# Kernel optimization log

Measured on AMD Instinct MI355X. Metric: run time of the kernel, lower is better.

The kernel has to match this reference:

```python
import jax, jax.numpy as jnp
import numpy as np
from jax import lax

B, T = 8, 32
D, H, W = 32, 32, 32
V = D * H * W
NPTS = 400          # nonzero events scattered per frame (<= K)
K = 512             # candidate cap (upper bound on nonzeros per frame)
DIST_THR = 2.0      # distance_threshold
MAX_EVENTS = 100    # max_events


def setup_inputs() -> dict:
    key = jax.random.key(0)
    k1, k2, k3 = jax.random.split(key, 3)
    magnitude = jax.random.normal(k1, (B, T, D, H, W), dtype=jnp.float32)
    # sparse positive energy: scatter NPTS uniform values per frame
    idx = jax.random.randint(k2, (B, T, NPTS), 0, V)
    vals = jax.random.uniform(k3, (B, T, NPTS), minval=0.1, maxval=1.0, dtype=jnp.float32)
    energy = jnp.zeros((B, T, V), jnp.float32).at[
        jnp.arange(B)[:, None, None], jnp.arange(T)[None, :, None], idx
    ].set(vals).reshape(B, T, D, H, W)
    x = jnp.stack([energy, magnitude], axis=2)  # [B,T,2,D,H,W]
    return {"x": x}


def _nms_mask(energy_flat):
    """Greedy 3D NMS over nonzero voxels of one frame. Returns keep-mask over V voxels."""
    scores, idx = lax.top_k(energy_flat, K)          # descending; all nonzeros are in top-K
    valid = scores > 0                               # top_k fill beyond nonzeros has score 0
    z = idx // (H * W)
    y = (idx // W) % H
    xx = idx % W
    coords = jnp.stack([z, y, xx], axis=-1).astype(jnp.float32)  # [K,3]
    ar = jnp.arange(K)

    def body(keep, i):
        active = keep[i] & valid[i]
        dist = jnp.sqrt(((coords[i] - coords) ** 2).sum(-1))
        suppress = active & (ar > i) & (dist < DIST_THR)
        return keep & ~suppress, None

    keep, _ = lax.scan(body, jnp.ones(K, bool), ar)
    keep = keep & valid
    # if more than max_events kept, drop everything past sorted index max_events
    keep = jnp.where(keep.sum() > MAX_EVENTS, keep & (ar < MAX_EVENTS), keep)
    mask = jnp.zeros_like(energy_flat).at[idx].add(keep.astype(energy_flat.dtype))
    return mask  # [V] in {0,1}


def _filter_frame(frame):
    # frame: [2, D, H, W]
    e = frame[0].reshape(V)
    mask = _nms_mask(e).reshape(1, D, H, W)
    has_points = jnp.any(e != 0)
    # empty frame passes through unchanged (original appends x[b,t] as-is)
    return jnp.where(has_points, frame * mask, frame)


def reference(x) -> jnp.ndarray:
    b, t = x.shape[:2]
    frames = x.reshape(b * t, 2, D, H, W)
    out = jax.vmap(_filter_frame)(frames)
    return out.reshape(x.shape)
```

## Files before the change

### kernel.cpp

```cpp
#include <hip/hip_runtime.h>
#include <stdint.h>

typedef unsigned long long u64;
typedef unsigned int u32;

#define VOX     32768
#define KCAP    512
#define MAXEV   100
#define NBRCAP  26
#define K1_BPF  8
#define K1_THREADS 256
#define K2_THREADS 512
#define CNT_STRIDE 16


__global__ __launch_bounds__(K1_THREADS) void stage_kernel(
    const float* __restrict__ x, float* __restrict__ out,
    int* __restrict__ gcnt, int* __restrict__ gnz, u64* __restrict__ grec)
{
    const int bid = blockIdx.x;
    const int f   = bid / K1_BPF;
    const int c   = bid % K1_BPF;
    const int tid = threadIdx.x;

    __shared__ u64 sbuf[KCAP];
    __shared__ int s_cnt, s_nz, s_base;

    if (tid == 0) { s_cnt = 0; s_nz = 0; }
    __syncthreads();

    {
        float4* o4 = (float4*)(out + (size_t)f * 2 * VOX) + c * (2 * VOX / K1_BPF / 4);
        const float4 z = make_float4(0.f, 0.f, 0.f, 0.f);
        #pragma unroll
        for (int h = 0; h < (2 * VOX / K1_BPF / 4) / K1_THREADS; ++h)
            o4[tid + h * K1_THREADS] = z;
    }

    const float4* e4 = (const float4*)(x + (size_t)f * 2 * VOX) + c * (VOX / K1_BPF / 4);
    bool anynz = false;
    #pragma unroll
    for (int h = 0; h < (VOX / K1_BPF / 4) / K1_THREADS; ++h) {
        int li = tid + h * K1_THREADS;
        float4 v = e4[li];
        int vbase = c * (VOX / K1_BPF) + li * 4;
        float vv[4] = {v.x, v.y, v.z, v.w};
        #pragma unroll
        for (int cc = 0; cc < 4; ++cc) {
            float val = vv[cc];
            anynz |= (val != 0.f);
            if (val > 0.f) {
                int slot = atomicAdd(&s_cnt, 1);
                if (slot < KCAP) {
                    int vox = vbase + cc;
                    sbuf[slot] = ((u64)__float_as_uint(val) << 32) | (u64)(~(u32)vox);
                }
            }
        }
    }
    if (anynz) s_nz = 1;
    __syncthreads();

    const int cnt = min(s_cnt, KCAP);
    if (tid == 0) {
        if (cnt) s_base = atomicAdd(&gcnt[f * CNT_STRIDE], cnt);
        if (s_nz) gnz[f] = 1;
    }
    __syncthreads();

    if (cnt) {
        const int base = s_base;
        for (int i = tid; i < cnt; i += K1_THREADS) {
            int o = base + i;
            if (o < KCAP) grec[f * KCAP + o] = sbuf[i];
        }
    }
}

__global__ __launch_bounds__(K2_THREADS) void nms_scatter_kernel(
    const float* __restrict__ x, float* __restrict__ out,
    const int* __restrict__ gcnt, const int* __restrict__ gnz,
    const u64* __restrict__ grec)
{
    const int f   = blockIdx.x;
    const int tid = threadIdx.x;

    __shared__ unsigned short smap[VOX];
    __shared__ u64   skey[KCAP];
    __shared__ short srank[KCAP];
    __shared__ unsigned char status[KCAP];
    __shared__ unsigned short pnbr[KCAP * NBRCAP];
    __shared__ int s_nkept, s_undec;

    const int n  = min(gcnt[f * CNT_STRIDE], KCAP);
    const int nz = gnz[f];

    if (nz == 0) {
        const float4* x4 = (const float4*)(x + (size_t)f * 2 * VOX);
        float4*       o4 = (float4*)(out + (size_t)f * 2 * VOX);
        for (int i = tid; i < 2 * VOX / 4; i += K2_THREADS) o4[i] = x4[i];
        return;
    }

    if (tid == 0) s_nkept = 0;
    {
        u32* m32 = (u32*)smap;
        #pragma unroll
        for (int h = 0; h < VOX / 2 / K2_THREADS; ++h)
            m32[tid + h * K2_THREADS] = 0xFFFFFFFFu;
    }
    __syncthreads();

    if (tid < n) {
        u64 k = grec[f * KCAP + tid];
        skey[tid] = k;
        smap[(int)(~(u32)k) & (VOX - 1)] = (unsigned short)tid;
    }
    __syncthreads();

    int pcnt = 0;
    if (tid < n) {
        const u64 kt = skey[tid];
        int rank = 0;
        #pragma unroll 8
        for (int i = 0; i < n; ++i)
            rank += (skey[i] > kt);
        srank[tid] = (short)rank;

        const int vox = (int)(~(u32)kt) & (VOX - 1);
        const int zt = vox >> 10, yt = (vox >> 5) & 31, xt = vox & 31;
        #pragma unroll
        for (int dz = -1; dz <= 1; ++dz) {
            int z = zt + dz; if ((unsigned)z >= 32) continue;
            #pragma unroll
            for (int dy = -1; dy <= 1; ++dy) {
                int yy = yt + dy; if ((unsigned)yy >= 32) continue;
                #pragma unroll
                for (int dx = -1; dx <= 1; ++dx) {
                    int xx = xt + dx; if ((unsigned)xx >= 32) continue;
                    int nv = (z << 10) | (yy << 5) | xx;
                    if (nv == vox) continue;
                    unsigned short m = smap[nv];
                    if (m != 0xFFFFu && skey[m] > kt)
                        pnbr[tid * NBRCAP + pcnt++] = m;
                }
            }
        }
        status[tid] = (pcnt == 0) ? (unsigned char)1 : (unsigned char)0;
    }
    __syncthreads();

    for (int round = 0; round < KCAP; ++round) {
        if (tid == 0) s_undec = 0;
        __syncthreads();
        if (tid < n && status[tid] == 0) {
            bool anyKept = false, anyUndec = false;
            for (int p = 0; p < pcnt; ++p) {
                unsigned char s = status[pnbr[tid * NBRCAP + p]];
                anyKept  |= (s == 1);
                anyUndec |= (s == 0);
            }
            if (anyKept)        status[tid] = 2;
            else if (!anyUndec) status[tid] = 1;
            else                s_undec = 1;
        }
        __syncthreads();
        if (s_undec == 0) break;
    }

    if (tid < n && status[tid] == 1) atomicAdd(&s_nkept, 1);
    __syncthreads();
    const int nkept = s_nkept;
    if (tid < n && status[tid] == 1 &&
        !(nkept > MAXEV && srank[tid] >= MAXEV)) {
        u64 k = skey[tid];
        int   vox = (int)(~(u32)k) & (VOX - 1);
        float val = __uint_as_float((u32)(k >> 32));
        float* of = out + (size_t)f * 2 * VOX;
        of[vox]       = val;
        of[VOX + vox] = x[(size_t)f * 2 * VOX + VOX + vox];
    }
}

extern "C" void kernel_launch(void* const* d_in, const int* in_sizes, int n_in,
                              void* d_out, int out_size, void* d_ws, size_t ws_size,
                              hipStream_t stream) {
    const float* x = (const float*)d_in[0];
    float* out = (float*)d_out;
    int frames = in_sizes[0] / (2 * VOX);

    int* gcnt = (int*)d_ws;
    int* gnz  = (int*)((char*)d_ws + 16384);
    u64* grec = (u64*)((char*)d_ws + 32768);

    hipMemsetAsync(d_ws, 0, 17408, stream);
    stage_kernel<<<frames * K1_BPF, K1_THREADS, 0, stream>>>(x, out, gcnt, gnz, grec);
    nms_scatter_kernel<<<frames, K2_THREADS, 0, stream>>>(x, out, gcnt, gnz, grec);
}
```

Baseline: 126.1 us.

## Replace global atomic compaction with per-block segments and drop memset

Each stage block now writes its candidates into a private fixed-size segment and records its own count and nonzero flag, instead of atomically reserving space in a shared per-frame buffer. The NMS kernel prefix-sums the eight segment counts and gathers segments per wavefront into shared memory. This removes the global atomics and the separate hipMemsetAsync launch. The cost is a larger workspace and a short serial prefix sum in the second kernel, and candidate order now follows block order rather than atomic arrival order.

```diff
diff --git a/kernel.cpp b/kernel.cpp
--- a/kernel.cpp
+++ b/kernel.cpp
@@ -11,7 +11,7 @@
 #define K1_BPF  8
 #define K1_THREADS 256
 #define K2_THREADS 512
-#define CNT_STRIDE 16
+#define SEGCAP  512
 
 
 __global__ __launch_bounds__(K1_THREADS) void stage_kernel(
@@ -23,8 +23,8 @@
     const int c   = bid % K1_BPF;
     const int tid = threadIdx.x;
 
-    __shared__ u64 sbuf[KCAP];
-    __shared__ int s_cnt, s_nz, s_base;
+    __shared__ u64 sbuf[SEGCAP];
+    __shared__ int s_cnt, s_nz;
 
     if (tid == 0) { s_cnt = 0; s_nz = 0; }
     __syncthreads();
@@ -51,7 +51,7 @@
             anynz |= (val != 0.f);
             if (val > 0.f) {
                 int slot = atomicAdd(&s_cnt, 1);
-                if (slot < KCAP) {
+                if (slot < SEGCAP) {
                     int vox = vbase + cc;
                     sbuf[slot] = ((u64)__float_as_uint(val) << 32) | (u64)(~(u32)vox);
                 }
@@ -61,19 +61,12 @@
     if (anynz) s_nz = 1;
     __syncthreads();
 
-    const int cnt = min(s_cnt, KCAP);
+    const int cnt = min(s_cnt, SEGCAP);
+    for (int i = tid; i < cnt; i += K1_THREADS)
+        grec[((size_t)f * K1_BPF + c) * SEGCAP + i] = sbuf[i];
     if (tid == 0) {
-        if (cnt) s_base = atomicAdd(&gcnt[f * CNT_STRIDE], cnt);
-        if (s_nz) gnz[f] = 1;
-    }
-    __syncthreads();
-
-    if (cnt) {
-        const int base = s_base;
-        for (int i = tid; i < cnt; i += K1_THREADS) {
-            int o = base + i;
-            if (o < KCAP) grec[f * KCAP + o] = sbuf[i];
-        }
+        gcnt[f * K1_BPF + c] = cnt;
+        gnz [f * K1_BPF + c] = s_nz;
     }
 }
 
@@ -82,39 +75,60 @@
     const int* __restrict__ gcnt, const int* __restrict__ gnz,
     const u64* __restrict__ grec)
 {
-    const int f   = blockIdx.x;
-    const int tid = threadIdx.x;
+    const int f    = blockIdx.x;
+    const int tid  = threadIdx.x;
+    const int wave = tid >> 6;
+    const int lane = tid & 63;
 
     __shared__ unsigned short smap[VOX];
     __shared__ u64   skey[KCAP];
     __shared__ short srank[KCAP];
     __shared__ unsigned char status[KCAP];
     __shared__ unsigned short pnbr[KCAP * NBRCAP];
-    __shared__ int s_nkept, s_undec;
-
-    const int n  = min(gcnt[f * CNT_STRIDE], KCAP);
-    const int nz = gnz[f];
-
-    if (nz == 0) {
+    __shared__ int s_off[K1_BPF + 1];
+    __shared__ int s_nz, s_nkept, s_undec;
+
+    if (tid == 0) {
+        int acc = 0, nz = 0;
+        #pragma unroll
+        for (int c = 0; c < K1_BPF; ++c) {
+            s_off[c] = acc;
+            acc += gcnt[f * K1_BPF + c];
+            nz  |= gnz [f * K1_BPF + c];
+        }
+        s_off[K1_BPF] = acc;
+        s_nz = nz;
+        s_nkept = 0;
+    }
+    {
+        u32* m32 = (u32*)smap;
+        #pragma unroll
+        for (int h = 0; h < VOX / 2 / K2_THREADS; ++h)
+            m32[tid + h * K2_THREADS] = 0xFFFFFFFFu;
+    }
+    __syncthreads();
+
+    const int n = min(s_off[K1_BPF], KCAP);
+
+    if (s_nz == 0) {
         const float4* x4 = (const float4*)(x + (size_t)f * 2 * VOX);
         float4*       o4 = (float4*)(out + (size_t)f * 2 * VOX);
         for (int i = tid; i < 2 * VOX / 4; i += K2_THREADS) o4[i] = x4[i];
         return;
     }
 
-    if (tid == 0) s_nkept = 0;
     {
-        u32* m32 = (u32*)smap;
-        #pragma unroll
-        for (int h = 0; h < VOX / 2 / K2_THREADS; ++h)
-            m32[tid + h * K2_THREADS] = 0xFFFFFFFFu;
-    }
-    __syncthreads();
-
-    if (tid < n) {
-        u64 k = grec[f * KCAP + tid];
-        skey[tid] = k;
-        smap[(int)(~(u32)k) & (VOX - 1)] = (unsigned short)tid;
+        const int cnt  = s_off[wave + 1] - s_off[wave];
+        const int base = s_off[wave];
+        const u64* seg = grec + ((size_t)f * K1_BPF + wave) * SEGCAP;
+        for (int i = lane; i < cnt; i += 64) {
+            int o = base + i;
+            if (o < KCAP) {
+                u64 k = seg[i];
+                skey[o] = k;
+                smap[(int)(~(u32)k) & (VOX - 1)] = (unsigned short)o;
+            }
+        }
     }
     __syncthreads();
 
@@ -190,10 +204,9 @@
     int frames = in_sizes[0] / (2 * VOX);
 
     int* gcnt = (int*)d_ws;
-    int* gnz  = (int*)((char*)d_ws + 16384);
-    u64* grec = (u64*)((char*)d_ws + 32768);
-
-    hipMemsetAsync(d_ws, 0, 17408, stream);
+    int* gnz  = (int*)((char*)d_ws + 65536);
+    u64* grec = (u64*)((char*)d_ws + 131072);
+
     stage_kernel<<<frames * K1_BPF, K1_THREADS, 0, stream>>>(x, out, gcnt, gnz, grec);
     nms_scatter_kernel<<<frames, K2_THREADS, 0, stream>>>(x, out, gcnt, gnz, grec);
 }
```

After: 122.6 us. -2.7%, faster.
